# Optimization experiments

Measured on AMD Instinct MI355X. Metric: run time of the kernel, lower is better.

Reference implementation:

```python
import jax, jax.numpy as jnp
import numpy as np

N_NODES = 100000
N_EDGES = 1600000
IN_CH = 165


def setup_inputs() -> dict:
    key = jax.random.key(0)
    ks = jax.random.split(key, 6)
    x = jax.random.normal(ks[0], (N_NODES, IN_CH), dtype=jnp.float32)
    edge_index = jax.random.randint(ks[1], (2, N_EDGES), 0, N_NODES, dtype=jnp.int32)
    # Glorot-ish init for weights
    W1 = jax.random.normal(ks[2], (IN_CH, 128), dtype=jnp.float32) * (1.0 / np.sqrt(IN_CH))
    b1 = jnp.zeros((128,), dtype=jnp.float32)
    W2 = jax.random.normal(ks[3], (128, 64), dtype=jnp.float32) * (1.0 / np.sqrt(128))
    b2 = jnp.zeros((64,), dtype=jnp.float32)
    Wo = jax.random.normal(ks[4], (64, 2), dtype=jnp.float32) * (1.0 / np.sqrt(64))
    bo = jnp.zeros((2,), dtype=jnp.float32)
    return {"x": x, "edge_index": edge_index, "W1": W1, "b1": b1,
            "W2": W2, "b2": b2, "Wo": Wo, "bo": bo}


def _gcn_norm(edge_index, n_nodes, dtype):
    """Add self-loops and compute symmetric normalization deg^-1/2 * deg^-1/2 (PyG gcn_norm)."""
    loops = jnp.arange(n_nodes, dtype=edge_index.dtype)
    ei = jnp.concatenate([edge_index, jnp.stack([loops, loops])], axis=1)
    row, col = ei[0], ei[1]
    deg = jax.ops.segment_sum(jnp.ones(ei.shape[1], dtype), col, num_segments=n_nodes)
    deg_inv_sqrt = jnp.where(deg > 0, jax.lax.rsqrt(deg), 0.0)
    norm = deg_inv_sqrt[row] * deg_inv_sqrt[col]  # [E+N]
    return row, col, norm


def _gcn_conv(h, row, col, norm, W, b, n_nodes):
    # transform first (F_in -> F_out), then gather-scale-scatter aggregate
    m = h @ W                                   # [N, F_out]
    msg = m[row] * norm[:, None]                # [E+N, F_out]
    agg = jax.ops.segment_sum(msg, col, num_segments=n_nodes)
    return agg + b


def reference(x, edge_index, W1, b1, W2, b2, Wo, bo):
    n_nodes = x.shape[0]
    row, col, norm = _gcn_norm(edge_index, n_nodes, x.dtype)
    h = jax.nn.relu(_gcn_conv(x, row, col, norm, W1, b1, n_nodes))
    h = jax.nn.relu(_gcn_conv(h, row, col, norm, W2, b2, n_nodes))
    return h @ Wo + bo  # [N, 2] logits
```

## Files before the change

### kernel.cpp

```cpp
#include <hip/hip_runtime.h>

#define N_NODES 100000
#define N_EDGES 1600000
#define IN_CH   165
#define BSHIFT 7
#define NBUCK  ((N_NODES + 127) / 128)
#define BCAP   3072
#define PA_BLOCKS 196

typedef unsigned short ushort_t;
typedef _Float16 f16;
typedef _Float16 f16x8 __attribute__((ext_vector_type(8)));
typedef _Float16 hfrag8 __attribute__((ext_vector_type(8)));
typedef short bfrag8 __attribute__((ext_vector_type(8)));
typedef float f32x4 __attribute__((ext_vector_type(4)));

__device__ __forceinline__ ushort_t f2bf(float f) {
    unsigned u = __float_as_uint(f);
    unsigned r = (u + 0x7fffu + ((u >> 16) & 1u)) >> 16;
    return (ushort_t)r;
}
__device__ __forceinline__ float bf2f(ushort_t h) {
    return __uint_as_float(((unsigned)h) << 16);
}

__device__ __forceinline__ void fmix_lo(float& a, unsigned pair, float s) {
    asm("v_fma_mix_f32 %0, %1, %2, %0 op_sel_hi:[1,0,0]" : "+v"(a) : "v"(pair), "v"(s));
}
__device__ __forceinline__ void fmix_hi(float& a, unsigned pair, float s) {
    asm("v_fma_mix_f32 %0, %1, %2, %0 op_sel:[1,0,0] op_sel_hi:[1,0,0]" : "+v"(a) : "v"(pair), "v"(s));
}
__device__ __forceinline__ void fmix_acc8(float* acc, uint4 v, float s) {
    fmix_lo(acc[0], v.x, s); fmix_hi(acc[1], v.x, s);
    fmix_lo(acc[2], v.y, s); fmix_hi(acc[3], v.y, s);
    fmix_lo(acc[4], v.z, s); fmix_hi(acc[5], v.z, s);
    fmix_lo(acc[6], v.w, s); fmix_hi(acc[7], v.w, s);
}

__global__ void wsplit_kernel(const float* __restrict__ W1, const float* __restrict__ W2,
                              ushort_t* __restrict__ wt1h, ushort_t* __restrict__ wt1l,
                              ushort_t* __restrict__ wt2h, ushort_t* __restrict__ wt2l) {
    int i = blockIdx.x * 256 + threadIdx.x;
    if (i < 128 * 192) {
        int ch = i / 192, k = i - ch * 192;
        float v = (k < IN_CH) ? W1[(size_t)k * 128 + ch] : 0.f;
        ushort_t h = f2bf(v);
        wt1h[i] = h;
        wt1l[i] = f2bf(v - bf2f(h));
    } else if (i < 128 * 192 + 64 * 128) {
        int j = i - 128 * 192;
        int ch = j / 128, k = j - ch * 128;
        float v = W2[(size_t)k * 64 + ch];
        f16 h = (f16)v;
        f16 l = (f16)(v - (float)h);
        wt2h[j] = *(ushort_t*)&h;
        wt2l[j] = *(ushort_t*)&l;
    }
}

__launch_bounds__(256)
__global__ void l1_kernel(const int* __restrict__ row, const int* __restrict__ col,
                          int* __restrict__ bfill, unsigned* __restrict__ tmp,
                          const float* __restrict__ X,
                          const ushort_t* __restrict__ wth, const ushort_t* __restrict__ wtl,
                          f16* __restrict__ M, int n_nodes) {
    __shared__ char smem[30720];
    int t = threadIdx.x;
    if (blockIdx.x < PA_BLOCKS) {
        int* lcnt = (int*)smem;
        int* lcur = ((int*)smem) + NBUCK;
        int e0 = (int)((long)blockIdx.x * N_EDGES / PA_BLOCKS);
        int e1 = (int)((long)(blockIdx.x + 1) * N_EDGES / PA_BLOCKS);
        for (int i = t; i < NBUCK; i += 256) lcnt[i] = 0;
        __syncthreads();
        for (int e = e0 + t; e < e1; e += 256)
            atomicAdd(&lcnt[col[e] >> BSHIFT], 1);
        __syncthreads();
        for (int b = t; b < NBUCK; b += 256) {
            int c = lcnt[b];
            lcur[b] = (c > 0) ? (b * BCAP + atomicAdd(&bfill[b], c)) : 0;
        }
        __syncthreads();
        for (int e = e0 + t; e < e1; e += 256) {
            int cc = col[e];
            int b = cc >> BSHIFT;
            int p = atomicAdd(&lcur[b], 1);
            tmp[p] = ((unsigned)(cc & 127) << 17) | (unsigned)row[e];
        }
    } else {
        constexpr int NOUT = 128, KTOT = 165, KPAD = 192;
        constexpr int NCT = NOUT / 16;
        constexpr int NCHUNK = KPAD / 32;
        constexpr int XP = 40;
        ushort_t (*xsh)[XP] = (ushort_t(*)[XP])(smem);
        ushort_t (*xsl)[XP] = (ushort_t(*)[XP])(smem + 5120);
        ushort_t (*wsh)[XP] = (ushort_t(*)[XP])(smem + 10240);
        ushort_t (*wsl)[XP] = (ushort_t(*)[XP])(smem + 20480);

        int l = t & 63, wid = t >> 6;
        long node0 = (long)(blockIdx.x - PA_BLOCKS) * 64;
        int arow = wid * 16 + (l & 15);
        int kq = (l >> 4) * 8;

        f32x4 acc[NCT];
        #pragma unroll
        for (int ct = 0; ct < NCT; ++ct) acc[ct] = (f32x4){0.f, 0.f, 0.f, 0.f};

        float xa[4], xb[4];
        bfrag8 wfh[2], wfl[2];

        auto loadX = [&](int c) {
            int k0 = c * 32;
            #pragma unroll
            for (int i = 0; i < 4; ++i) {
                int idx = t + i * 256;
                int node = idx >> 4, kp = idx & 15;
                long g = node0 + node;
                int k = k0 + 2 * kp;
                bool ok = (g < n_nodes);
                xa[i] = (ok && k < KTOT) ? X[g * KTOT + k] : 0.f;
                xb[i] = (ok && k + 1 < KTOT) ? X[g * KTOT + k + 1] : 0.f;
            }
        };
        auto loadW = [&](int c) {
            int k0 = c * 32;
            #pragma unroll
            for (int i = 0; i < 2; ++i) {
                int idx = t + i * 256;
                int ch = idx >> 2, q = idx & 3;
                wfh[i] = *(const bfrag8*)&wth[(size_t)ch * KPAD + k0 + q * 8];
                wfl[i] = *(const bfrag8*)&wtl[(size_t)ch * KPAD + k0 + q * 8];
            }
        };
        auto storeLDS = [&]() {
            #pragma unroll
            for (int i = 0; i < 4; ++i) {
                int idx = t + i * 256;
                int node = idx >> 4, kp = idx & 15;
                ushort_t ha = (ushort_t)(__float_as_uint(xa[i]) >> 16);
                ushort_t la = f2bf(xa[i] - bf2f(ha));
                ushort_t hb = (ushort_t)(__float_as_uint(xb[i]) >> 16);
                ushort_t lb = f2bf(xb[i] - bf2f(hb));
                *(unsigned*)&xsh[node][2 * kp] = (unsigned)ha | ((unsigned)hb << 16);
                *(unsigned*)&xsl[node][2 * kp] = (unsigned)la | ((unsigned)lb << 16);
            }
            #pragma unroll
            for (int i = 0; i < 2; ++i) {
                int idx = t + i * 256;
                int ch = idx >> 2, q = idx & 3;
                *(bfrag8*)&wsh[ch][q * 8] = wfh[i];
                *(bfrag8*)&wsl[ch][q * 8] = wfl[i];
            }
        };

        loadX(0); loadW(0);
        for (int c = 0; c < NCHUNK; ++c) {
            storeLDS();
            __syncthreads();
            if (c + 1 < NCHUNK) { loadX(c + 1); loadW(c + 1); }
            bfrag8 ah = *(const bfrag8*)&xsh[arow][kq];
            bfrag8 al = *(const bfrag8*)&xsl[arow][kq];
            #pragma unroll
            for (int ct = 0; ct < NCT; ++ct) {
                bfrag8 bh = *(const bfrag8*)&wsh[ct * 16 + (l & 15)][kq];
                bfrag8 bl = *(const bfrag8*)&wsl[ct * 16 + (l & 15)][kq];
                acc[ct] = __builtin_amdgcn_mfma_f32_16x16x32_bf16(ah, bh, acc[ct], 0, 0, 0);
                acc[ct] = __builtin_amdgcn_mfma_f32_16x16x32_bf16(ah, bl, acc[ct], 0, 0, 0);
                acc[ct] = __builtin_amdgcn_mfma_f32_16x16x32_bf16(al, bh, acc[ct], 0, 0, 0);
            }
            __syncthreads();
        }

        int nl = wid * 16 + (l >> 4) * 4;
        #pragma unroll
        for (int ct = 0; ct < NCT; ++ct) {
            int ch = ct * 16 + (l & 15);
            #pragma unroll
            for (int j = 0; j < 4; ++j) {
                long node = node0 + nl + j;
                if (node < n_nodes)
                    M[node * NOUT + ch] = (f16)acc[ct][j];
            }
        }
    }
}

__global__ void prep_kernel(const unsigned* __restrict__ tmp, const int* __restrict__ bfill,
                            int* __restrict__ cnt, int* __restrict__ bbase,
                            int* __restrict__ off) {
    __shared__ int lcnt[128];
    __shared__ int ssc[256];
    int b = blockIdx.x, t = threadIdx.x;
    if (t < 128) lcnt[t] = 0;
    __syncthreads();
    int total = min(bfill[b], BCAP);
    const unsigned* reg = tmp + (size_t)b * BCAP;
    for (int i = t; i < total; i += 256)
        atomicAdd(&lcnt[(reg[i] >> 17) & 127], 1);
    __syncthreads();
    if (t < 128) {
        int n = (b << BSHIFT) + t;
        if (n < N_NODES) cnt[n] = lcnt[t];
    }
    if (b == 0) {
        int v[4]; int run = 0;
        int base = t * 4;
        #pragma unroll
        for (int j = 0; j < 4; ++j) {
            int c = (base + j < NBUCK) ? bfill[base + j] : 0;
            v[j] = run; run += c;
        }
        ssc[t] = run;
        __syncthreads();
        for (int o = 1; o < 256; o <<= 1) {
            int x = (t >= o) ? ssc[t - o] : 0;
            __syncthreads();
            ssc[t] += x;
            __syncthreads();
        }
        int prev = (t > 0) ? ssc[t - 1] : 0;
        #pragma unroll
        for (int j = 0; j < 4; ++j)
            if (base + j < NBUCK) bbase[base + j] = prev + v[j];
        if (t == 0) off[N_NODES] = N_EDGES;
    }
}

__global__ void bucketB2_kernel(const unsigned* __restrict__ tmp, const int* __restrict__ bfill,
                                const int* __restrict__ bbase, const int* __restrict__ cnt,
                                int* __restrict__ off, unsigned* __restrict__ srt) {
    __shared__ int sh[128];
    __shared__ int lcur[128];
    int b = blockIdx.x, t = threadIdx.x;
    int nb0 = b << BSHIFT;
    int base = bbase[b];
    if (t < 128) {
        int n = nb0 + t;
        sh[t] = (n < N_NODES) ? cnt[n] : 0;
    }
    __syncthreads();
    for (int o = 1; o < 128; o <<= 1) {
        int x = (t < 128 && t >= o) ? sh[t - o] : 0;
        __syncthreads();
        if (t < 128) sh[t] += x;
        __syncthreads();
    }
    if (t < 128) {
        int excl = (t > 0) ? sh[t - 1] : 0;
        int n = nb0 + t;
        if (n < N_NODES) off[n] = base + excl;
        lcur[t] = excl;
    }
    __syncthreads();
    int total = min(bfill[b], BCAP);
    const unsigned* reg = tmp + (size_t)b * BCAP;
    for (int i = t; i < total; i += 256) {
        unsigned e = reg[i];
        int c = (e >> 17) & 127;
        unsigned src = e & 0x1FFFFu;
        unsigned cs = min((unsigned)cnt[src], 255u);
        int p = atomicAdd(&lcur[c], 1);
        srt[base + p] = (cs << 17) | src;
    }
}

__launch_bounds__(256)
__global__ void mfma_gemm2_kernel(const f16* __restrict__ X,
                                  const ushort_t* __restrict__ wth,
                                  const ushort_t* __restrict__ wtl,
                                  f16* __restrict__ M, int n_nodes) {
    constexpr int NOUT = 64, KTOT = 128;
    constexpr int NCT = NOUT / 16;
    constexpr int NCHUNK = KTOT / 32;
    constexpr int XP = 40;
    __shared__ ushort_t xs[64][XP];
    __shared__ ushort_t wsh[NOUT][XP];
    __shared__ ushort_t wsl[NOUT][XP];

    int t = threadIdx.x;
    int l = t & 63, wid = t >> 6;
    long node0 = (long)blockIdx.x * 64;

    int arow = wid * 16 + (l & 15);
    int kq = (l >> 4) * 8;

    f32x4 acc[NCT];
    #pragma unroll
    for (int ct = 0; ct < NCT; ++ct) acc[ct] = (f32x4){0.f, 0.f, 0.f, 0.f};

    unsigned xu[4];
    bfrag8 wfh, wfl;

    auto loadX = [&](int c) {
        int k0 = c * 32;
        #pragma unroll
        for (int i = 0; i < 4; ++i) {
            int idx = t + i * 256;
            int node = idx >> 4, kp = idx & 15;
            long g = node0 + node;
            xu[i] = (g < n_nodes) ? *(const unsigned*)&X[g * KTOT + k0 + 2 * kp] : 0u;
        }
    };
    auto loadW = [&](int c) {
        int k0 = c * 32;
        int ch = t >> 2, q = t & 3;
        wfh = *(const bfrag8*)&wth[(size_t)ch * KTOT + k0 + q * 8];
        wfl = *(const bfrag8*)&wtl[(size_t)ch * KTOT + k0 + q * 8];
    };
    auto storeLDS = [&]() {
        #pragma unroll
        for (int i = 0; i < 4; ++i) {
            int idx = t + i * 256;
            int node = idx >> 4, kp = idx & 15;
            *(unsigned*)&xs[node][2 * kp] = xu[i];
        }
        int ch = t >> 2, q = t & 3;
        *(bfrag8*)&wsh[ch][q * 8] = wfh;
        *(bfrag8*)&wsl[ch][q * 8] = wfl;
    };

    loadX(0); loadW(0);
    for (int c = 0; c < NCHUNK; ++c) {
        storeLDS();
        __syncthreads();
        if (c + 1 < NCHUNK) { loadX(c + 1); loadW(c + 1); }
        hfrag8 a = *(const hfrag8*)&xs[arow][kq];
        #pragma unroll
        for (int ct = 0; ct < NCT; ++ct) {
            hfrag8 bh = *(const hfrag8*)&wsh[ct * 16 + (l & 15)][kq];
            hfrag8 bl = *(const hfrag8*)&wsl[ct * 16 + (l & 15)][kq];
            acc[ct] = __builtin_amdgcn_mfma_f32_16x16x32_f16(a, bh, acc[ct], 0, 0, 0);
            acc[ct] = __builtin_amdgcn_mfma_f32_16x16x32_f16(a, bl, acc[ct], 0, 0, 0);
        }
        __syncthreads();
    }

    int nl = wid * 16 + (l >> 4) * 4;
    #pragma unroll
    for (int ct = 0; ct < NCT; ++ct) {
        int ch = ct * 16 + (l & 15);
        #pragma unroll
        for (int j = 0; j < 4; ++j) {
            long node = node0 + nl + j;
            if (node < n_nodes)
                M[node * NOUT + ch] = (f16)acc[ct][j];
        }
    }
}

__global__ void agg1_kernel(const f16* __restrict__ ms, const unsigned* __restrict__ srt,
                            const int* __restrict__ off,
                            const float* __restrict__ b1, f16* __restrict__ h1) {
    int wave = threadIdx.x >> 6;
    int lane = threadIdx.x & 63;
    int n = blockIdx.x * 4 + wave;
    if (n >= N_NODES) return;
    int g = lane >> 4, p = lane & 15;
    const char* msb = (const char*)ms;
    unsigned pb = (unsigned)p * 16;
    int s0 = off[n], s1 = off[n + 1];
    float dn = rsqrtf((float)(s1 - s0) + 1.f);
    float acc[8] = {0.f, 0.f, 0.f, 0.f, 0.f, 0.f, 0.f, 0.f};
    if (g == 0) {
        uint4 v = *(const uint4*)(msb + (unsigned)n * 256 + pb);
        fmix_acc8(acc, v, dn);
    }
    unsigned sv = (s0 + lane < s1) ? srt[s0 + lane] : 0;
    for (int base = s0; base < s1; base += 64) {
        int nb2 = base + 64;
        unsigned svn = (nb2 + lane < s1) ? srt[nb2 + lane] : 0;
        int cnt_ = min(64, s1 - base);
        int j = 0;
        for (; j + 15 < cnt_; j += 16) {
            unsigned e0 = (unsigned)__shfl((int)sv, j + g);
            unsigned e1 = (unsigned)__shfl((int)sv, j + 4 + g);
            unsigned e2 = (unsigned)__shfl((int)sv, j + 8 + g);
            unsigned e3 = (unsigned)__shfl((int)sv, j + 12 + g);
            uint4 v0 = *(const uint4*)(msb + (e0 & 0x1FFFFu) * 256 + pb);
            uint4 v1 = *(const uint4*)(msb + (e1 & 0x1FFFFu) * 256 + pb);
            uint4 v2 = *(const uint4*)(msb + (e2 & 0x1FFFFu) * 256 + pb);
            uint4 v3 = *(const uint4*)(msb + (e3 & 0x1FFFFu) * 256 + pb);
            float d0 = rsqrtf((float)(e0 >> 17) + 1.f);
            float d1 = rsqrtf((float)(e1 >> 17) + 1.f);
            float d2 = rsqrtf((float)(e2 >> 17) + 1.f);
            float d3 = rsqrtf((float)(e3 >> 17) + 1.f);
            fmix_acc8(acc, v0, d0);
            fmix_acc8(acc, v1, d1);
            fmix_acc8(acc, v2, d2);
            fmix_acc8(acc, v3, d3);
        }
        for (; j < cnt_; j += 4) {
            unsigned e = (unsigned)__shfl((int)sv, j + g);
            float ws = (j + g < cnt_) ? rsqrtf((float)(e >> 17) + 1.f) : 0.f;
            uint4 v = *(const uint4*)(msb + (e & 0x1FFFFu) * 256 + pb);
            fmix_acc8(acc, v, ws);
        }
        sv = svn;
    }
    #pragma unroll
    for (int i = 0; i < 8; ++i) {
        acc[i] += __shfl_xor(acc[i], 16);
        acc[i] += __shfl_xor(acc[i], 32);
    }
    if (lane < 16) {
        float4 ba = ((const float4*)b1)[lane * 2];
        float4 bb = ((const float4*)b1)[lane * 2 + 1];
        float bv[8] = {ba.x, ba.y, ba.z, ba.w, bb.x, bb.y, bb.z, bb.w};
        f16x8 r;
        #pragma unroll
        for (int i = 0; i < 8; ++i)
            r[i] = (f16)fmaxf(acc[i] * dn + bv[i], 0.f);
        *(f16x8*)(h1 + (size_t)n * 128 + lane * 8) = r;
    }
}

__global__ void agg2_kernel(const f16* __restrict__ ms, const unsigned* __restrict__ srt,
                            const int* __restrict__ off,
                            const float* __restrict__ b2, const float* __restrict__ Wo,
                            const float* __restrict__ bo, float* __restrict__ out) {
    int wave = threadIdx.x >> 6;
    int lane = threadIdx.x & 63;
    int n = blockIdx.x * 4 + wave;
    if (n >= N_NODES) return;
    int g = lane >> 3, p = lane & 7;
    const char* msb = (const char*)ms;
    unsigned pb = (unsigned)p * 16;
    int s0 = off[n], s1 = off[n + 1];
    float dn = rsqrtf((float)(s1 - s0) + 1.f);
    float acc[8] = {0.f, 0.f, 0.f, 0.f, 0.f, 0.f, 0.f, 0.f};
    if (g == 0) {
        uint4 v = *(const uint4*)(msb + (unsigned)n * 128 + pb);
        fmix_acc8(acc, v, dn);
    }
    unsigned sv = (s0 + lane < s1) ? srt[s0 + lane] : 0;
    for (int base = s0; base < s1; base += 64) {
        int nb2 = base + 64;
        unsigned svn = (nb2 + lane < s1) ? srt[nb2 + lane] : 0;
        int cnt_ = min(64, s1 - base);
        int j = 0;
        for (; j + 15 < cnt_; j += 16) {
            unsigned e0 = (unsigned)__shfl((int)sv, j + g);
            unsigned e1 = (unsigned)__shfl((int)sv, j + 8 + g);
            uint4 v0 = *(const uint4*)(msb + (e0 & 0x1FFFFu) * 128 + pb);
            uint4 v1 = *(const uint4*)(msb + (e1 & 0x1FFFFu) * 128 + pb);
            float d0 = rsqrtf((float)(e0 >> 17) + 1.f);
            float d1 = rsqrtf((float)(e1 >> 17) + 1.f);
            fmix_acc8(acc, v0, d0);
            fmix_acc8(acc, v1, d1);
        }
        for (; j < cnt_; j += 8) {
            unsigned e = (unsigned)__shfl((int)sv, j + g);
            float ws = (j + g < cnt_) ? rsqrtf((float)(e >> 17) + 1.f) : 0.f;
            uint4 v = *(const uint4*)(msb + (e & 0x1FFFFu) * 128 + pb);
            fmix_acc8(acc, v, ws);
        }
        sv = svn;
    }
    #pragma unroll
    for (int i = 0; i < 8; ++i) {
        acc[i] += __shfl_xor(acc[i], 8);
        acc[i] += __shfl_xor(acc[i], 16);
        acc[i] += __shfl_xor(acc[i], 32);
    }
    float p0 = 0.f, p1 = 0.f;
    #pragma unroll
    for (int i = 0; i < 8; ++i) {
        int ch = p * 8 + i;
        float hc = fmaxf(acc[i] * dn + b2[ch], 0.f);
        p0 = fmaf(hc, Wo[ch * 2], p0);
        p1 = fmaf(hc, Wo[ch * 2 + 1], p1);
    }
    p0 += __shfl_xor(p0, 1); p1 += __shfl_xor(p1, 1);
    p0 += __shfl_xor(p0, 2); p1 += __shfl_xor(p1, 2);
    p0 += __shfl_xor(p0, 4); p1 += __shfl_xor(p1, 4);
    if (lane == 0) {
        out[(size_t)n * 2]     = p0 + bo[0];
        out[(size_t)n * 2 + 1] = p1 + bo[1];
    }
}

extern "C" void kernel_launch(void* const* d_in, const int* in_sizes, int n_in,
                              void* d_out, int out_size, void* d_ws, size_t ws_size,
                              hipStream_t stream) {
    const float* x  = (const float*)d_in[0];
    const int*   ei = (const int*)d_in[1];
    const int*   row = ei;
    const int*   col = ei + N_EDGES;
    const float* W1 = (const float*)d_in[2];
    const float* b1 = (const float*)d_in[3];
    const float* W2 = (const float*)d_in[4];
    const float* b2 = (const float*)d_in[5];
    const float* Wo = (const float*)d_in[6];
    const float* bo = (const float*)d_in[7];
    float* out = (float*)d_out;

    char* base = (char*)d_ws;
    auto alloc = [&](size_t bytes) {
        char* p = base;
        base += (bytes + 255) & ~(size_t)255;
        return p;
    };
    int*      cnt  = (int*)alloc((size_t)N_NODES * 4);
    int*      off  = (int*)alloc((size_t)(N_NODES + 1) * 4);
    int*      bbase= (int*)alloc((size_t)(NBUCK + 1) * 4);
    int*      bfill= (int*)alloc((size_t)NBUCK * 4);
    unsigned* tmp  = (unsigned*)alloc((size_t)NBUCK * BCAP * 4 + 4096);
    unsigned* srt  = (unsigned*)alloc((size_t)N_EDGES * 4);
    f16*      m    = (f16*)alloc((size_t)N_NODES * 128 * 2);
    f16*      h1   = (f16*)alloc((size_t)N_NODES * 128 * 2);
    ushort_t* wt1h = (ushort_t*)alloc((size_t)128 * 192 * 2);
    ushort_t* wt1l = (ushort_t*)alloc((size_t)128 * 192 * 2);
    ushort_t* wt2h = (ushort_t*)alloc((size_t)64 * 128 * 2);
    ushort_t* wt2l = (ushort_t*)alloc((size_t)64 * 128 * 2);

    hipMemsetAsync(bfill, 0, (size_t)NBUCK * 4, stream);
    wsplit_kernel<<<(128 * 192 + 64 * 128 + 255) / 256, 256, 0, stream>>>(W1, W2, wt1h, wt1l, wt2h, wt2l);

    int gemm1_blocks = (N_NODES + 63) / 64;
    l1_kernel<<<PA_BLOCKS + gemm1_blocks, 256, 0, stream>>>(row, col, bfill, tmp,
                                                            x, wt1h, wt1l, m, N_NODES);
    prep_kernel<<<NBUCK, 256, 0, stream>>>(tmp, bfill, cnt, bbase, off);
    bucketB2_kernel<<<NBUCK, 256, 0, stream>>>(tmp, bfill, bbase, cnt, off, srt);

    agg1_kernel<<<(N_NODES + 3) / 4, 256, 0, stream>>>(m, srt, off, b1, h1);

    mfma_gemm2_kernel<<<(N_NODES + 63) / 64, 256, 0, stream>>>(h1, wt2h, wt2l, m, N_NODES);
    agg2_kernel<<<(N_NODES + 3) / 4, 256, 0, stream>>>(m, srt, off, b2, Wo, bo, out);
}
```

Baseline: 207.5 us.

## Regroup kernel fusion and drop LDS staging from both MFMA GEMMs

```diff
diff --git a/kernel.cpp b/kernel.cpp
--- a/kernel.cpp
+++ b/kernel.cpp
@@ -7,6 +7,8 @@
 #define NBUCK  ((N_NODES + 127) / 128)
 #define BCAP   3072
 #define PA_BLOCKS 196
+#define WSPLIT_BLOCKS 128
+#define G1_BLOCKS ((N_NODES + 63) / 64)
 
 typedef unsigned short ushort_t;
 typedef _Float16 f16;
@@ -37,192 +39,154 @@
     fmix_lo(acc[6], v.w, s); fmix_hi(acc[7], v.w, s);
 }
 
-__global__ void wsplit_kernel(const float* __restrict__ W1, const float* __restrict__ W2,
-                              ushort_t* __restrict__ wt1h, ushort_t* __restrict__ wt1l,
-                              ushort_t* __restrict__ wt2h, ushort_t* __restrict__ wt2l) {
-    int i = blockIdx.x * 256 + threadIdx.x;
-    if (i < 128 * 192) {
-        int ch = i / 192, k = i - ch * 192;
-        float v = (k < IN_CH) ? W1[(size_t)k * 128 + ch] : 0.f;
-        ushort_t h = f2bf(v);
-        wt1h[i] = h;
-        wt1l[i] = f2bf(v - bf2f(h));
-    } else if (i < 128 * 192 + 64 * 128) {
-        int j = i - 128 * 192;
-        int ch = j / 128, k = j - ch * 128;
-        float v = W2[(size_t)k * 64 + ch];
-        f16 h = (f16)v;
-        f16 l = (f16)(v - (float)h);
-        wt2h[j] = *(ushort_t*)&h;
-        wt2l[j] = *(ushort_t*)&l;
+__global__ void bucketA_kernel(const int* __restrict__ row, const int* __restrict__ col,
+                               int* __restrict__ bfill, unsigned* __restrict__ tmp,
+                               const float* __restrict__ W1, const float* __restrict__ W2,
+                               ushort_t* __restrict__ wt1h, ushort_t* __restrict__ wt1l,
+                               ushort_t* __restrict__ wt2h, ushort_t* __restrict__ wt2l) {
+    __shared__ int lcnt[NBUCK];
+    __shared__ int lcur[NBUCK];
+    int t = threadIdx.x;
+    if (blockIdx.x >= PA_BLOCKS) {
+        int i = (blockIdx.x - PA_BLOCKS) * 256 + t;
+        if (i < 128 * 192) {
+            int ch = i / 192, k = i - ch * 192;
+            float v = (k < IN_CH) ? W1[(size_t)k * 128 + ch] : 0.f;
+            ushort_t h = f2bf(v);
+            wt1h[i] = h;
+            wt1l[i] = f2bf(v - bf2f(h));
+        } else if (i < 128 * 192 + 64 * 128) {
+            int j = i - 128 * 192;
+            int ch = j / 128, k = j - ch * 128;
+            float v = W2[(size_t)k * 64 + ch];
+            f16 h = (f16)v;
+            f16 l = (f16)(v - (float)h);
+            wt2h[j] = *(ushort_t*)&h;
+            wt2l[j] = *(ushort_t*)&l;
+        }
+        return;
+    }
+    int e0 = (int)((long)blockIdx.x * N_EDGES / PA_BLOCKS);
+    int e1 = (int)((long)(blockIdx.x + 1) * N_EDGES / PA_BLOCKS);
+    for (int i = t; i < NBUCK; i += 256) lcnt[i] = 0;
+    __syncthreads();
+    for (int e = e0 + t; e < e1; e += 256)
+        atomicAdd(&lcnt[col[e] >> BSHIFT], 1);
+    __syncthreads();
+    for (int b = t; b < NBUCK; b += 256) {
+        int c = lcnt[b];
+        lcur[b] = (c > 0) ? (b * BCAP + atomicAdd(&bfill[b], c)) : 0;
+    }
+    __syncthreads();
+    for (int e = e0 + t; e < e1; e += 256) {
+        int cc = col[e];
+        int b = cc >> BSHIFT;
+        int p = atomicAdd(&lcur[b], 1);
+        tmp[p] = ((unsigned)(cc & 127) << 17) | (unsigned)row[e];
     }
 }
 
 __launch_bounds__(256)
-__global__ void l1_kernel(const int* __restrict__ row, const int* __restrict__ col,
-                          int* __restrict__ bfill, unsigned* __restrict__ tmp,
-                          const float* __restrict__ X,
-                          const ushort_t* __restrict__ wth, const ushort_t* __restrict__ wtl,
-                          f16* __restrict__ M, int n_nodes) {
-    __shared__ char smem[30720];
+__global__ void g1prep_kernel(const unsigned* __restrict__ tmp, const int* __restrict__ bfill,
+                              int* __restrict__ cnt, int* __restrict__ bbase, int* __restrict__ off,
+                              const float* __restrict__ X,
+                              const ushort_t* __restrict__ wth, const ushort_t* __restrict__ wtl,
+                              f16* __restrict__ M, int n_nodes) {
+    __shared__ int lcnt[128];
+    __shared__ int ssc[256];
     int t = threadIdx.x;
-    if (blockIdx.x < PA_BLOCKS) {
-        int* lcnt = (int*)smem;
-        int* lcur = ((int*)smem) + NBUCK;
-        int e0 = (int)((long)blockIdx.x * N_EDGES / PA_BLOCKS);
-        int e1 = (int)((long)(blockIdx.x + 1) * N_EDGES / PA_BLOCKS);
-        for (int i = t; i < NBUCK; i += 256) lcnt[i] = 0;
+    if (blockIdx.x < NBUCK) {
+        int b = blockIdx.x;
+        if (t < 128) lcnt[t] = 0;
         __syncthreads();
-        for (int e = e0 + t; e < e1; e += 256)
-            atomicAdd(&lcnt[col[e] >> BSHIFT], 1);
+        int total = min(bfill[b], BCAP);
+        const unsigned* reg = tmp + (size_t)b * BCAP;
+        for (int i = t; i < total; i += 256)
+            atomicAdd(&lcnt[(reg[i] >> 17) & 127], 1);
         __syncthreads();
-        for (int b = t; b < NBUCK; b += 256) {
-            int c = lcnt[b];
-            lcur[b] = (c > 0) ? (b * BCAP + atomicAdd(&bfill[b], c)) : 0;
-        }
-        __syncthreads();
-        for (int e = e0 + t; e < e1; e += 256) {
-            int cc = col[e];
-            int b = cc >> BSHIFT;
-            int p = atomicAdd(&lcur[b], 1);
-            tmp[p] = ((unsigned)(cc & 127) << 17) | (unsigned)row[e];
-        }
-    } else {
-        constexpr int NOUT = 128, KTOT = 165, KPAD = 192;
-        constexpr int NCT = NOUT / 16;
-        constexpr int NCHUNK = KPAD / 32;
-        constexpr int XP = 40;
-        ushort_t (*xsh)[XP] = (ushort_t(*)[XP])(smem);
-        ushort_t (*xsl)[XP] = (ushort_t(*)[XP])(smem + 5120);
-        ushort_t (*wsh)[XP] = (ushort_t(*)[XP])(smem + 10240);
-        ushort_t (*wsl)[XP] = (ushort_t(*)[XP])(smem + 20480);
-
-        int l = t & 63, wid = t >> 6;
-        long node0 = (long)(blockIdx.x - PA_BLOCKS) * 64;
-        int arow = wid * 16 + (l & 15);
-        int kq = (l >> 4) * 8;
-
-        f32x4 acc[NCT];
-        #pragma unroll
-        for (int ct = 0; ct < NCT; ++ct) acc[ct] = (f32x4){0.f, 0.f, 0.f, 0.f};
-
-        float xa[4], xb[4];
-        bfrag8 wfh[2], wfl[2];
-
-        auto loadX = [&](int c) {
-            int k0 = c * 32;
-            #pragma unroll
-            for (int i = 0; i < 4; ++i) {
-                int idx = t + i * 256;
-                int node = idx >> 4, kp = idx & 15;
-                long g = node0 + node;
-                int k = k0 + 2 * kp;
-                bool ok = (g < n_nodes);
-                xa[i] = (ok && k < KTOT) ? X[g * KTOT + k] : 0.f;
-                xb[i] = (ok && k + 1 < KTOT) ? X[g * KTOT + k + 1] : 0.f;
-            }
-        };
-        auto loadW = [&](int c) {
-            int k0 = c * 32;
-            #pragma unroll
-            for (int i = 0; i < 2; ++i) {
-                int idx = t + i * 256;
-                int ch = idx >> 2, q = idx & 3;
-                wfh[i] = *(const bfrag8*)&wth[(size_t)ch * KPAD + k0 + q * 8];
-                wfl[i] = *(const bfrag8*)&wtl[(size_t)ch * KPAD + k0 + q * 8];
-            }
-        };
-        auto storeLDS = [&]() {
-            #pragma unroll
-            for (int i = 0; i < 4; ++i) {
-                int idx = t + i * 256;
-                int node = idx >> 4, kp = idx & 15;
-                ushort_t ha = (ushort_t)(__float_as_uint(xa[i]) >> 16);
-                ushort_t la = f2bf(xa[i] - bf2f(ha));
-                ushort_t hb = (ushort_t)(__float_as_uint(xb[i]) >> 16);
-                ushort_t lb = f2bf(xb[i] - bf2f(hb));
-                *(unsigned*)&xsh[node][2 * kp] = (unsigned)ha | ((unsigned)hb << 16);
-                *(unsigned*)&xsl[node][2 * kp] = (unsigned)la | ((unsigned)lb << 16);
-            }
-            #pragma unroll
-            for (int i = 0; i < 2; ++i) {
-                int idx = t + i * 256;
-                int ch = idx >> 2, q = idx & 3;
-                *(bfrag8*)&wsh[ch][q * 8] = wfh[i];
-                *(bfrag8*)&wsl[ch][q * 8] = wfl[i];
-            }
-        };
-
-        loadX(0); loadW(0);
-        for (int c = 0; c < NCHUNK; ++c) {
-            storeLDS();
-            __syncthreads();
-            if (c + 1 < NCHUNK) { loadX(c + 1); loadW(c + 1); }
-            bfrag8 ah = *(const bfrag8*)&xsh[arow][kq];
-            bfrag8 al = *(const bfrag8*)&xsl[arow][kq];
-            #pragma unroll
-            for (int ct = 0; ct < NCT; ++ct) {
-                bfrag8 bh = *(const bfrag8*)&wsh[ct * 16 + (l & 15)][kq];
-                bfrag8 bl = *(const bfrag8*)&wsl[ct * 16 + (l & 15)][kq];
-                acc[ct] = __builtin_amdgcn_mfma_f32_16x16x32_bf16(ah, bh, acc[ct], 0, 0, 0);
-                acc[ct] = __builtin_amdgcn_mfma_f32_16x16x32_bf16(ah, bl, acc[ct], 0, 0, 0);
-                acc[ct] = __builtin_amdgcn_mfma_f32_16x16x32_bf16(al, bh, acc[ct], 0, 0, 0);
-            }
-            __syncthreads();
-        }
-
-        int nl = wid * 16 + (l >> 4) * 4;
-        #pragma unroll
-        for (int ct = 0; ct < NCT; ++ct) {
-            int ch = ct * 16 + (l & 15);
+        if (t < 128) {
+            int n = (b << BSHIFT) + t;
+            if (n < N_NODES) cnt[n] = lcnt[t];
+        }
+        if (b == 0) {
+            int v[4]; int run = 0;
+            int base = t * 4;
             #pragma unroll
             for (int j = 0; j < 4; ++j) {
-                long node = node0 + nl + j;
-                if (node < n_nodes)
-                    M[node * NOUT + ch] = (f16)acc[ct][j];
+                int c = (base + j < NBUCK) ? bfill[base + j] : 0;
+                v[j] = run; run += c;
             }
-        }
-    }
-}
-
-__global__ void prep_kernel(const unsigned* __restrict__ tmp, const int* __restrict__ bfill,
-                            int* __restrict__ cnt, int* __restrict__ bbase,
-                            int* __restrict__ off) {
-    __shared__ int lcnt[128];
-    __shared__ int ssc[256];
-    int b = blockIdx.x, t = threadIdx.x;
-    if (t < 128) lcnt[t] = 0;
-    __syncthreads();
-    int total = min(bfill[b], BCAP);
-    const unsigned* reg = tmp + (size_t)b * BCAP;
-    for (int i = t; i < total; i += 256)
-        atomicAdd(&lcnt[(reg[i] >> 17) & 127], 1);
-    __syncthreads();
-    if (t < 128) {
-        int n = (b << BSHIFT) + t;
-        if (n < N_NODES) cnt[n] = lcnt[t];
-    }
-    if (b == 0) {
-        int v[4]; int run = 0;
-        int base = t * 4;
+            ssc[t] = run;
+            __syncthreads();
+            for (int o = 1; o < 256; o <<= 1) {
+                int x = (t >= o) ? ssc[t - o] : 0;
+                __syncthreads();
+                ssc[t] += x;
+                __syncthreads();
+            }
+            int prev = (t > 0) ? ssc[t - 1] : 0;
+            #pragma unroll
+            for (int j = 0; j < 4; ++j)
+                if (base + j < NBUCK) bbase[base + j] = prev + v[j];
+            if (t == 0) off[N_NODES] = N_EDGES;
+        }
+        return;
+    }
+    int bid = blockIdx.x - NBUCK;
+    int l = t & 63, wid = t >> 6;
+    long node0 = (long)bid * 64;
+    int r = (int)node0 + wid * 16 + (l & 15);
+    int rr = min(r, n_nodes - 1);
+    int q = l >> 4;
+    const float* xrow = X + (size_t)rr * IN_CH;
+
+    f32x4 acc[8];
+    #pragma unroll
+    for (int ct = 0; ct < 8; ++ct) acc[ct] = (f32x4){0.f, 0.f, 0.f, 0.f};
+
+    #pragma unroll
+    for (int c = 0; c < 6; ++c) {
+        int k = c * 32 + q * 8;
+        float a[8];
+        if (c < 5) {
+            #pragma unroll
+            for (int i = 0; i < 8; ++i) a[i] = xrow[k + i];
+        } else {
+            #pragma unroll
+            for (int i = 0; i < 8; ++i) a[i] = 0.f;
+            if (q == 0) {
+                a[0] = xrow[160]; a[1] = xrow[161]; a[2] = xrow[162];
+                a[3] = xrow[163]; a[4] = xrow[164];
+            }
+        }
+        bfrag8 ah, al;
+        #pragma unroll
+        for (int i = 0; i < 8; ++i) {
+            ushort_t h = (ushort_t)(__float_as_uint(a[i]) >> 16);
+            ah[i] = (short)h;
+            al[i] = (short)f2bf(a[i] - bf2f(h));
+        }
+        #pragma unroll
+        for (int ct = 0; ct < 8; ++ct) {
+            int ch = ct * 16 + (l & 15);
+            bfrag8 bh = *(const bfrag8*)&wth[(size_t)ch * 192 + k];
+            bfrag8 bl = *(const bfrag8*)&wtl[(size_t)ch * 192 + k];
+            acc[ct] = __builtin_amdgcn_mfma_f32_16x16x32_bf16(ah, bh, acc[ct], 0, 0, 0);
+            acc[ct] = __builtin_amdgcn_mfma_f32_16x16x32_bf16(ah, bl, acc[ct], 0, 0, 0);
+            acc[ct] = __builtin_amdgcn_mfma_f32_16x16x32_bf16(al, bh, acc[ct], 0, 0, 0);
+        }
+    }
+
+    int nl = wid * 16 + (l >> 4) * 4;
+    #pragma unroll
+    for (int ct = 0; ct < 8; ++ct) {
+        int ch = ct * 16 + (l & 15);
         #pragma unroll
         for (int j = 0; j < 4; ++j) {
-            int c = (base + j < NBUCK) ? bfill[base + j] : 0;
-            v[j] = run; run += c;
-        }
-        ssc[t] = run;
-        __syncthreads();
-        for (int o = 1; o < 256; o <<= 1) {
-            int x = (t >= o) ? ssc[t - o] : 0;
-            __syncthreads();
-            ssc[t] += x;
-            __syncthreads();
-        }
-        int prev = (t > 0) ? ssc[t - 1] : 0;
-        #pragma unroll
-        for (int j = 0; j < 4; ++j)
-            if (base + j < NBUCK) bbase[base + j] = prev + v[j];
-        if (t == 0) off[N_NODES] = N_EDGES;
+            long node = node0 + nl + j;
+            if (node < n_nodes)
+                M[node * 128 + ch] = (f16)acc[ct][j];
+        }
     }
 }
 
@@ -265,85 +229,44 @@
 }
 
 __launch_bounds__(256)
-__global__ void mfma_gemm2_kernel(const f16* __restrict__ X,
-                                  const ushort_t* __restrict__ wth,
-                                  const ushort_t* __restrict__ wtl,
-                                  f16* __restrict__ M, int n_nodes) {
-    constexpr int NOUT = 64, KTOT = 128;
-    constexpr int NCT = NOUT / 16;
-    constexpr int NCHUNK = KTOT / 32;
-    constexpr int XP = 40;
-    __shared__ ushort_t xs[64][XP];
-    __shared__ ushort_t wsh[NOUT][XP];
-    __shared__ ushort_t wsl[NOUT][XP];
-
+__global__ void gemm2_kernel(const f16* __restrict__ H,
+                             const ushort_t* __restrict__ wth, const ushort_t* __restrict__ wtl,
+                             f16* __restrict__ M, int n_nodes) {
     int t = threadIdx.x;
     int l = t & 63, wid = t >> 6;
     long node0 = (long)blockIdx.x * 64;
-
-    int arow = wid * 16 + (l & 15);
-    int kq = (l >> 4) * 8;
-
-    f32x4 acc[NCT];
-    #pragma unroll
-    for (int ct = 0; ct < NCT; ++ct) acc[ct] = (f32x4){0.f, 0.f, 0.f, 0.f};
-
-    unsigned xu[4];
-    bfrag8 wfh, wfl;
-
-    auto loadX = [&](int c) {
-        int k0 = c * 32;
-        #pragma unroll
-        for (int i = 0; i < 4; ++i) {
-            int idx = t + i * 256;
-            int node = idx >> 4, kp = idx & 15;
-            long g = node0 + node;
-            xu[i] = (g < n_nodes) ? *(const unsigned*)&X[g * KTOT + k0 + 2 * kp] : 0u;
-        }
-    };
-    auto loadW = [&](int c) {
-        int k0 = c * 32;
-        int ch = t >> 2, q = t & 3;
-        wfh = *(const bfrag8*)&wth[(size_t)ch * KTOT + k0 + q * 8];
-        wfl = *(const bfrag8*)&wtl[(size_t)ch * KTOT + k0 + q * 8];
-    };
-    auto storeLDS = [&]() {
-        #pragma unroll
-        for (int i = 0; i < 4; ++i) {
-            int idx = t + i * 256;
-            int node = idx >> 4, kp = idx & 15;
-            *(unsigned*)&xs[node][2 * kp] = xu[i];
-        }
-        int ch = t >> 2, q = t & 3;
-        *(bfrag8*)&wsh[ch][q * 8] = wfh;
-        *(bfrag8*)&wsl[ch][q * 8] = wfl;
-    };
-
-    loadX(0); loadW(0);
-    for (int c = 0; c < NCHUNK; ++c) {
-        storeLDS();
-        __syncthreads();
-        if (c + 1 < NCHUNK) { loadX(c + 1); loadW(c + 1); }
-        hfrag8 a = *(const hfrag8*)&xs[arow][kq];
-        #pragma unroll
-        for (int ct = 0; ct < NCT; ++ct) {
-            hfrag8 bh = *(const hfrag8*)&wsh[ct * 16 + (l & 15)][kq];
-            hfrag8 bl = *(const hfrag8*)&wsl[ct * 16 + (l & 15)][kq];
+    int r = (int)node0 + wid * 16 + (l & 15);
+    int rr = min(r, n_nodes - 1);
+    int q = l >> 4;
+    const f16* hrow = H + (size_t)rr * 128;
+
+    f32x4 acc[4];
+    #pragma unroll
+    for (int ct = 0; ct < 4; ++ct) acc[ct] = (f32x4){0.f, 0.f, 0.f, 0.f};
+
+    #pragma unroll
+    for (int c = 0; c < 4; ++c) {
+        int k = c * 32 + q * 8;
+        hfrag8 a = *(const hfrag8*)&hrow[k];
+        #pragma unroll
+        for (int ct = 0; ct < 4; ++ct) {
+            int ch = ct * 16 + (l & 15);
+            hfrag8 bh = *(const hfrag8*)&wth[(size_t)ch * 128 + k];
+            hfrag8 bl = *(const hfrag8*)&wtl[(size_t)ch * 128 + k];
             acc[ct] = __builtin_amdgcn_mfma_f32_16x16x32_f16(a, bh, acc[ct], 0, 0, 0);
             acc[ct] = __builtin_amdgcn_mfma_f32_16x16x32_f16(a, bl, acc[ct], 0, 0, 0);
         }
-        __syncthreads();
     }
 
     int nl = wid * 16 + (l >> 4) * 4;
     #pragma unroll
-    for (int ct = 0; ct < NCT; ++ct) {
+    for (int ct = 0; ct < 4; ++ct) {
         int ch = ct * 16 + (l & 15);
         #pragma unroll
         for (int j = 0; j < 4; ++j) {
             long node = node0 + nl + j;
             if (node < n_nodes)
-                M[node * NOUT + ch] = (f16)acc[ct][j];
+                M[node * 64 + ch] = (f16)acc[ct][j];
         }
     }
 }
@@ -514,16 +437,17 @@
     ushort_t* wt2l = (ushort_t*)alloc((size_t)64 * 128 * 2);
 
     hipMemsetAsync(bfill, 0, (size_t)NBUCK * 4, stream);
-    wsplit_kernel<<<(128 * 192 + 64 * 128 + 255) / 256, 256, 0, stream>>>(W1, W2, wt1h, wt1l, wt2h, wt2l);
-
-    int gemm1_blocks = (N_NODES + 63) / 64;
-    l1_kernel<<<PA_BLOCKS + gemm1_blocks, 256, 0, stream>>>(row, col, bfill, tmp,
-                                                            x, wt1h, wt1l, m, N_NODES);
-    prep_kernel<<<NBUCK, 256, 0, stream>>>(tmp, bfill, cnt, bbase, off);
+
+    bucketA_kernel<<<PA_BLOCKS + WSPLIT_BLOCKS, 256, 0, stream>>>(
+        row, col, bfill, tmp, W1, W2, wt1h, wt1l, wt2h, wt2l);
+
+    g1prep_kernel<<<NBUCK + G1_BLOCKS, 256, 0, stream>>>(
+        tmp, bfill, cnt, bbase, off, x, wt1h, wt1l, m, N_NODES);
+
     bucketB2_kernel<<<NBUCK, 256, 0, stream>>>(tmp, bfill, bbase, cnt, off, srt);
 
     agg1_kernel<<<(N_NODES + 3) / 4, 256, 0, stream>>>(m, srt, off, b1, h1);
 
-    mfma_gemm2_kernel<<<(N_NODES + 63) / 64, 256, 0, stream>>>(h1, wt2h, wt2l, m, N_NODES);
+    gemm2_kernel<<<G1_BLOCKS, 256, 0, stream>>>(h1, wt2h, wt2l, m, N_NODES);
     agg2_kernel<<<(N_NODES + 3) / 4, 256, 0, stream>>>(m, srt, off, b2, Wo, bo, out);
 }
```

New measurement: 290.1 us. 1.4x slower.
